# Optimization experiments

Measured on AMD Instinct MI355X. Metric: run time of the kernel, lower is better.

## Reference

```python
import jax, jax.numpy as jnp
import numpy as np

H = 1024
V = 5000
NUM_LAYERS = 2
B, T, U = 2, 128, 64


def setup_inputs() -> dict:
    key = jax.random.key(0)
    ks = jax.random.split(key, 16)
    s = 0.02
    inp = {
        "encoder_out": jax.random.normal(ks[0], (B, T, H), dtype=jnp.float32),
        "targets": jax.random.randint(ks[1], (B, U), 0, V),
        "embed": jax.random.normal(ks[2], (V, H), dtype=jnp.float32) * s,
        # stacked 2-layer LSTM params, PyTorch gate order (i, f, g, o)
        "lstm_Wih": jax.random.normal(ks[3], (NUM_LAYERS, 4 * H, H), dtype=jnp.float32) * s,
        "lstm_Whh": jax.random.normal(ks[4], (NUM_LAYERS, 4 * H, H), dtype=jnp.float32) * s,
        "lstm_bih": jnp.zeros((NUM_LAYERS, 4 * H), dtype=jnp.float32),
        "lstm_bhh": jnp.zeros((NUM_LAYERS, 4 * H), dtype=jnp.float32),
        "enc_W": jax.random.normal(ks[5], (H, H), dtype=jnp.float32) * s,
        "enc_b": jnp.zeros((H,), dtype=jnp.float32),
        "pred_W": jax.random.normal(ks[6], (H, H), dtype=jnp.float32) * s,
        "pred_b": jnp.zeros((H,), dtype=jnp.float32),
        "out_W": jax.random.normal(ks[7], (V + 1, H), dtype=jnp.float32) * s,
        "out_b": jnp.zeros((V + 1,), dtype=jnp.float32),
    }
    return inp


def _lstm_layer(x, Wih, Whh, bih, bhh):
    # x: [B, U, H] -> [B, U, H]; single LSTM layer, PyTorch gate order i,f,g,o
    b, u, h = x.shape
    bias = bih + bhh  # [4H]
    # precompute input projections for all timesteps: [U, B, 4H]
    xg = jnp.einsum('buh,gh->ubg', x, Wih) + bias

    def step(carry, xt):
        hprev, cprev = carry
        gates = xt + hprev @ Whh.T  # [B, 4H]
        i, f, g, o = jnp.split(gates, 4, axis=-1)
        i = jax.nn.sigmoid(i)
        f = jax.nn.sigmoid(f)
        g = jnp.tanh(g)
        o = jax.nn.sigmoid(o)
        c = f * cprev + i * g
        hnew = o * jnp.tanh(c)
        return (hnew, c), hnew

    init = (jnp.zeros((b, h), x.dtype), jnp.zeros((b, h), x.dtype))
    _, hs = jax.lax.scan(step, init, xg)  # hs: [U, B, H]
    return hs.transpose(1, 0, 2)


def reference(encoder_out, targets, embed, lstm_Wih, lstm_Whh, lstm_bih, lstm_bhh,
              enc_W, enc_b, pred_W, pred_b, out_W, out_b):
    # Prediction network: embedding + 2-layer LSTM (deterministic -> no dropout)
    x = embed[targets]  # [B, U, H]
    for l in range(NUM_LAYERS):
        x = _lstm_layer(x, lstm_Wih[l], lstm_Whh[l], lstm_bih[l], lstm_bhh[l])
    pred_out = x  # [B, U, H]

    # Joint network: proj + broadcast add over (T, U) + ReLU + output linear
    enc_p = jnp.einsum('bth,oh->bto', encoder_out, enc_W) + enc_b  # [B, T, H]
    prd_p = jnp.einsum('buh,oh->buo', pred_out, pred_W) + pred_b    # [B, U, H]
    joint = jax.nn.relu(enc_p[:, :, None, :] + prd_p[:, None, :, :])  # [B, T, U, H]
    logits = jnp.einsum('btuh,vh->btuv', joint, out_W) + out_b  # [B, T, U, V+1]
    return logits
```

## Files before the change

kernel.cpp:

```cpp
#include <hip/hip_runtime.h>
#include <hip/hip_bf16.h>

#define B_ 2
#define T_ 128
#define U_ 64
#define H_ 1024
#define NO_ 5001

typedef __attribute__((ext_vector_type(8))) short bf16x8;
typedef __attribute__((ext_vector_type(4))) float f32x4;

__device__ __forceinline__ float bf2f(unsigned short s) {
  unsigned int u = ((unsigned int)s) << 16;
  float f; __builtin_memcpy(&f, &u, 4); return f;
}
__device__ __forceinline__ unsigned short f2bf(float f) {
  unsigned int u; __builtin_memcpy(&u, &f, 4);
  u = u + 0x7FFFu + ((u >> 16) & 1u);
  return (unsigned short)(u >> 16);
}
__device__ __forceinline__ float fsig(float x) {
  x = fminf(fmaxf(x, -30.f), 30.f);
  float e = __expf(-x);
  return __builtin_amdgcn_rcpf(1.f + e);
}
__device__ __forceinline__ float ftanh(float x) {
  x = fminf(fmaxf(x, -15.f), 15.f);
  float e = __expf(2.f * x);
  return (e - 1.f) * __builtin_amdgcn_rcpf(e + 1.f);
}

__device__ __forceinline__ void gload_lds16(const unsigned short* g, unsigned short* l) {
  __builtin_amdgcn_global_load_lds(
      (const __attribute__((address_space(1))) unsigned int*)g,
      (__attribute__((address_space(3))) unsigned int*)l,
      16, 0, 0);
}

#define R_OUTW 1280256
#define R_WIH  (R_OUTW + 2097152)
#define R_WHH  (R_WIH + 2097152)
#define R_ENCW (R_WHH + 262144)
#define R_PRDW (R_ENCW + 262144)
#define R_ENC  (R_PRDW + 65536)
#define R_BIAS (R_ENC + 1280)
#define R_EMB  (R_BIAS + 32768)

__global__ void k_cvt_all(
    const float* __restrict__ outW, const float* __restrict__ Wih,
    const float* __restrict__ Whh,  const float* __restrict__ encW,
    const float* __restrict__ prdW, const float* __restrict__ enc,
    const float* __restrict__ outB,
    const int* __restrict__ tg, const float* __restrict__ em,
    unsigned short* __restrict__ outW_bf, unsigned short* __restrict__ Wih_bf,
    unsigned short* __restrict__ Whh_bf,  unsigned short* __restrict__ encW_bf,
    unsigned short* __restrict__ prdW_bf, unsigned short* __restrict__ enc_bf,
    float* __restrict__ biasPad, unsigned short* __restrict__ x0_bf)
{
  int i = blockIdx.x * 256 + threadIdx.x;
  const float* src; unsigned short* dst; int off;
  if (i < R_OUTW)      { src = outW; dst = outW_bf; off = i; }
  else if (i < R_WIH)  { src = Wih;  dst = Wih_bf;  off = i - R_OUTW; }
  else if (i < R_WHH)  { src = Whh;  dst = Whh_bf;  off = i - R_WIH; }
  else if (i < R_ENCW) { src = encW; dst = encW_bf; off = i - R_WHH; }
  else if (i < R_PRDW) { src = prdW; dst = prdW_bf; off = i - R_ENCW; }
  else if (i < R_ENC)  { src = enc;  dst = enc_bf;  off = i - R_PRDW; }
  else if (i < R_BIAS) {
    int e0 = (i - R_ENC) * 4;
    float4 v;
    v.x = (e0 + 0 < NO_) ? outB[e0 + 0] : 0.f;
    v.y = (e0 + 1 < NO_) ? outB[e0 + 1] : 0.f;
    v.z = (e0 + 2 < NO_) ? outB[e0 + 2] : 0.f;
    v.w = (e0 + 3 < NO_) ? outB[e0 + 3] : 0.f;
    *(float4*)&biasPad[e0] = v;
    return;
  } else {
    int idx = i - R_BIAS;
    int bu = idx >> 8;
    int kc = (idx & 255) << 2;
    int t = tg[bu];
    const float4 v = *(const float4*)&em[(long)t * H_ + kc];
    ushort4 o; o.x = f2bf(v.x); o.y = f2bf(v.y); o.z = f2bf(v.z); o.w = f2bf(v.w);
    *(ushort4*)&x0_bf[bu * H_ + kc] = o;
    return;
  }
  const float4 v = ((const float4*)src)[off];
  ushort4 o;
  o.x = f2bf(v.x); o.y = f2bf(v.y); o.z = f2bf(v.z); o.w = f2bf(v.w);
  ((ushort4*)dst)[off] = o;
}

__global__ __launch_bounds__(256) void gemm_proj(
    const unsigned short* __restrict__ enc_bf, const unsigned short* __restrict__ x2_bf,
    const unsigned short* __restrict__ encW_bf, const unsigned short* __restrict__ prdW_bf,
    const float* __restrict__ encB, const float* __restrict__ prdB,
    float* __restrict__ ep, float* __restrict__ pp)
{
  __shared__ unsigned short As[128 * 32];
  __shared__ unsigned short Bs[128 * 32];
  const int tid = threadIdx.x;
  const unsigned short* A; const unsigned short* W; const float* b1; float* C;
  int m0;
  if (blockIdx.y < 2) { A = enc_bf; W = encW_bf; b1 = encB; C = ep; m0 = blockIdx.y * 128; }
  else                { A = x2_bf;  W = prdW_bf; b1 = prdB; C = pp; m0 = 0; }
  const int n0 = blockIdx.x * 128;
  const int K = H_, N = H_;
  const int lane = tid & 63, w = tid >> 6;
  const int wr = (w >> 1) * 64, wc = (w & 1) * 64;
  const int lr = lane & 15, lk = (lane >> 4) * 8;
  f32x4 acc[4][4] = {};

  for (int k0 = 0; k0 < K; k0 += 32) {
#pragma unroll
    for (int s = 0; s < 2; ++s) {
      int idx = (w * 2 + s) * 64 + lane;
      int row = idx >> 2, c8 = (idx & 3) * 8;
      gload_lds16(&A[(long)(m0 + row) * K + k0 + c8], &As[(w * 2 + s) * 512]);
      gload_lds16(&W[(long)(n0 + row) * K + k0 + c8], &Bs[(w * 2 + s) * 512]);
    }
    __syncthreads();
    bf16x8 aF[4], bF[4];
#pragma unroll
    for (int i = 0; i < 4; ++i) {
      aF[i] = *(const bf16x8*)&As[(wr + i * 16 + lr) * 32 + lk];
      bF[i] = *(const bf16x8*)&Bs[(wc + i * 16 + lr) * 32 + lk];
    }
#pragma unroll
    for (int i = 0; i < 4; ++i)
#pragma unroll
      for (int j = 0; j < 4; ++j)
        acc[i][j] = __builtin_amdgcn_mfma_f32_16x16x32_bf16(aF[i], bF[j], acc[i][j], 0, 0, 0);
    __syncthreads();
  }

  const int lq = (lane >> 4) * 4;
#pragma unroll
  for (int j = 0; j < 4; ++j) {
    int col = n0 + wc + j * 16 + lr;
    float bb = b1[col];
#pragma unroll
    for (int i = 0; i < 4; ++i) {
      int rowg = m0 + wr + i * 16 + lq;
#pragma unroll
      for (int r = 0; r < 4; ++r)
        C[(long)(rowg + r) * N + col] = acc[i][j][r] + bb;
    }
  }
}

#define STAGE_A(kt2, kh, rb) \
  gload_lds16(aSrc[rb] + (kt2) * 64 + (kh) * 32, \
              &As_f[((((kt2) & 1) * 2 + (kh)) * 8192) + ((rb) * 128 + wv * 16) * 32])
#define STAGE_B(kt2, kh, rb) \
  gload_lds16(bSrc[rb] + (kt2) * 64 + (kh) * 32, \
              &Bs_f[((((kt2) & 1) * 2 + (kh)) * 8192) + ((rb) * 128 + wv * 16) * 32])

__global__ __launch_bounds__(512, 1) void gemm_logits(
    const unsigned short* __restrict__ A, const unsigned short* __restrict__ W,
    const float* __restrict__ biasPad, float* __restrict__ C, int M, int N, int K)
{
  __shared__ __align__(16) unsigned short lds_all[65536];
  unsigned short* As_f = lds_all;
  unsigned short* Bs_f = lds_all + 32768;
  const int tid = threadIdx.x;
  const int lane = tid & 63, wv = tid >> 6;
  const int wm = wv >> 2, wn = wv & 3;
  int swzb = (blockIdx.x & 7) * 160 + (blockIdx.x >> 3);
  const int n0 = (swzb >> 6) * 256;
  const int m0 = (swzb & 63) * 256;
  const int NT = K / 64;

  const unsigned short* aSrc[2];
  const unsigned short* bSrc[2];
#pragma unroll
  for (int rb = 0; rb < 2; ++rb) {
    int rl = rb * 128 + (tid >> 2);
    int c2s = (tid & 3) ^ ((rl >> 1) & 3);
    aSrc[rb] = A + (long)(m0 + rl) * K + c2s * 8;
    bSrc[rb] = W + (long)(n0 + rl) * K + c2s * 8;
  }
  int aOff[8], bOff[4];
#pragma unroll
  for (int i = 0; i < 8; ++i) {
    int r = wm * 128 + i * 16 + (lane & 15);
    aOff[i] = r * 32 + (((lane >> 4) ^ ((r >> 1) & 3)) * 8);
  }
#pragma unroll
  for (int j = 0; j < 4; ++j) {
    int r = wn * 64 + j * 16 + (lane & 15);
    bOff[j] = r * 32 + (((lane >> 4) ^ ((r >> 1) & 3)) * 8);
  }

  f32x4 acc[8][4] = {};

  STAGE_A(0, 0, 0); STAGE_A(0, 0, 1); STAGE_B(0, 0, 0); STAGE_B(0, 0, 1);
  STAGE_A(0, 1, 0); STAGE_A(0, 1, 1); STAGE_B(0, 1, 0); STAGE_B(0, 1, 1);

  for (int kt = 0; kt < NT; ++kt) {
    const int b = kt & 1;
    asm volatile("s_waitcnt vmcnt(4)" ::: "memory");
    __builtin_amdgcn_s_barrier();
    __builtin_amdgcn_sched_barrier(0);
    {
      const int base = (b * 2 + 0) * 8192;
      bf16x8 aF[8], bF[4];
#pragma unroll
      for (int i = 0; i < 8; ++i) aF[i] = *(const bf16x8*)&As_f[base + aOff[i]];
#pragma unroll
      for (int j = 0; j < 4; ++j) bF[j] = *(const bf16x8*)&Bs_f[base + bOff[j]];
      if (kt + 1 < NT) {
        STAGE_A(kt + 1, 0, 0); STAGE_A(kt + 1, 0, 1);
        STAGE_B(kt + 1, 0, 0); STAGE_B(kt + 1, 0, 1);
        STAGE_A(kt + 1, 1, 0); STAGE_A(kt + 1, 1, 1);
      }
      __builtin_amdgcn_s_setprio(1);
#pragma unroll
      for (int i = 0; i < 8; ++i)
#pragma unroll
        for (int j = 0; j < 4; ++j)
          acc[i][j] = __builtin_amdgcn_mfma_f32_16x16x32_bf16(aF[i], bF[j], acc[i][j], 0, 0, 0);
      __builtin_amdgcn_s_setprio(0);
    }
    if (kt + 1 < NT) { asm volatile("s_waitcnt vmcnt(6)" ::: "memory"); }
    else             { asm volatile("s_waitcnt vmcnt(0)" ::: "memory"); }
    __builtin_amdgcn_s_barrier();
    __builtin_amdgcn_sched_barrier(0);
    {
      const int base = (b * 2 + 1) * 8192;
      bf16x8 aF[8], bF[4];
#pragma unroll
      for (int i = 0; i < 8; ++i) aF[i] = *(const bf16x8*)&As_f[base + aOff[i]];
#pragma unroll
      for (int j = 0; j < 4; ++j) bF[j] = *(const bf16x8*)&Bs_f[base + bOff[j]];
      if (kt + 1 < NT) { STAGE_B(kt + 1, 1, 0); STAGE_B(kt + 1, 1, 1); }
      __builtin_amdgcn_s_setprio(1);
#pragma unroll
      for (int i = 0; i < 8; ++i)
#pragma unroll
        for (int j = 0; j < 4; ++j)
          acc[i][j] = __builtin_amdgcn_mfma_f32_16x16x32_bf16(aF[i], bF[j], acc[i][j], 0, 0, 0);
      __builtin_amdgcn_s_setprio(0);
    }
  }

  float* eb = (float*)lds_all;
  const int lq = (lane >> 4) * 4;
  float bv4[4];
#pragma unroll
  for (int j = 0; j < 4; ++j) bv4[j] = biasPad[n0 + wn * 64 + j * 16 + (lane & 15)];

#pragma unroll
  for (int cp = 0; cp < 4; ++cp) {
    __syncthreads();
#pragma unroll
    for (int ii = 0; ii < 2; ++ii) {
      int rbase = wm * 32 + ii * 16 + lq;
#pragma unroll
      for (int j = 0; j < 4; ++j) {
        int col = wn * 64 + j * 16 + (lane & 15);
#pragma unroll
        for (int r = 0; r < 4; ++r)
          eb[(rbase + r) * 261 + col] = acc[cp * 2 + ii][j][r] + bv4[j];
      }
    }
    __syncthreads();
    {
      int rl = tid >> 3, ci = tid & 7;
      long grow = (long)m0 + (rl >> 5) * 128 + cp * 32 + (rl & 31);
      float* crow = C + grow * N + n0;
      const float* er = &eb[rl * 261];
#pragma unroll
      for (int k = 0; k < 8; ++k) {
        int col = ci * 4 + k * 32;
        float4 v = *(const float4*)&er[col];
        int gc = n0 + col;
        if (gc + 4 <= N) {
          *(float4*)&crow[col] = v;
        } else if (gc < N) {
          float tmp[4] = {v.x, v.y, v.z, v.w};
#pragma unroll
          for (int e = 0; e < 4; ++e)
            if (gc + e < N) crow[col + e] = tmp[e];
        }
      }
    }
  }
}

__global__ void k_joint(const float* __restrict__ ep, const float* __restrict__ pp,
                        unsigned short* __restrict__ jt)
{
  int idx = blockIdx.x * 256 + threadIdx.x;
  int m = idx >> 8;
  int kc = (idx & 255) << 2;
  int erow = m >> 6;
  int prow = (m >> 13) * U_ + (m & 63);
  const float4 e = *(const float4*)&ep[erow * H_ + kc];
  const float4 p = *(const float4*)&pp[prow * H_ + kc];
  float4 s;
  s.x = fmaxf(e.x + p.x, 0.f); s.y = fmaxf(e.y + p.y, 0.f);
  s.z = fmaxf(e.z + p.z, 0.f); s.w = fmaxf(e.w + p.w, 0.f);
  ushort4 o; o.x = f2bf(s.x); o.y = f2bf(s.y); o.z = f2bf(s.z); o.w = f2bf(s.w);
  *(ushort4*)&jt[m * H_ + kc] = o;
}

__global__ __launch_bounds__(256, 1) void lstm_fused3(
    const unsigned short* __restrict__ x0_bf,
    const unsigned short* __restrict__ Whh0,
    const unsigned short* __restrict__ Wih0,
    const unsigned short* __restrict__ Whh1,
    const unsigned short* __restrict__ Wih1,
    const float* __restrict__ bih0, const float* __restrict__ bhh0,
    const float* __restrict__ bih1, const float* __restrict__ bhh1,
    unsigned short* __restrict__ x2_bf,
    float* __restrict__ hbuf0,
    float* __restrict__ hbuf1,
    float* __restrict__ xbuf,
    float* __restrict__ xg1buf, int* __restrict__ flags1,
    float* __restrict__ xg0buf, int* __restrict__ flags0)
{
  __shared__ float hs[2][H_];
  __shared__ float part[2][4][64][2];
  __shared__ float biasS[64];

  const int tid = threadIdx.x;
  const int grp = blockIdx.x >> 6;
  const int bid = blockIdx.x & 63;
  const int w = tid >> 6, l = tid & 63;
  const int g = l >> 4, q = l & 15;
  const int row = g * 1024 + bid * 16 + q;
  const int kb = w * 256;

#define DOT_BODY(WREG, SRC)                                                              \
  _Pragma("unroll")                                                                      \
  for (int it = 0; it < 32; ++it) {                                                      \
    bf16x8 wv = WREG[it];                                                                \
    float4 h0a = *(const float4*)&SRC[0][kb + it * 8];                                   \
    float4 h0b = *(const float4*)&SRC[0][kb + it * 8 + 4];                               \
    float4 h1a = *(const float4*)&SRC[1][kb + it * 8];                                   \
    float4 h1b = *(const float4*)&SRC[1][kb + it * 8 + 4];                               \
    a00 += bf2f((unsigned short)wv[0]) * h0a.x + bf2f((unsigned short)wv[4]) * h0b.x;    \
    a01 += bf2f((unsigned short)wv[1]) * h0a.y + bf2f((unsigned short)wv[5]) * h0b.y;    \
    a02 += bf2f((unsigned short)wv[2]) * h0a.z + bf2f((unsigned short)wv[6]) * h0b.z;    \
    a03 += bf2f((unsigned short)wv[3]) * h0a.w + bf2f((unsigned short)wv[7]) * h0b.w;    \
    a10 += bf2f((unsigned short)wv[0]) * h1a.x + bf2f((unsigned short)wv[4]) * h1b.x;    \
    a11 += bf2f((unsigned short)wv[1]) * h1a.y + bf2f((unsigned short)wv[5]) * h1b.y;    \
    a12 += bf2f((unsigned short)wv[2]) * h1a.z + bf2f((unsigned short)wv[6]) * h1b.z;    \
    a13 += bf2f((unsigned short)wv[3]) * h1a.w + bf2f((unsigned short)wv[7]) * h1b.w;    \
  }

  if (grp == 0 || grp == 2) {
    const unsigned short* Whh = (grp == 0) ? Whh0 : Whh1;
    float* hbuf   = (grp == 0) ? hbuf0 : hbuf1;
    const float* xgbufR = (grp == 0) ? xg0buf : xg1buf;
    const int* flagsR   = (grp == 0) ? flags0 : flags1;
    bf16x8 wreg[32];
#pragma unroll
    for (int it = 0; it < 32; ++it)
      wreg[it] = *(const bf16x8*)&Whh[(long)row * H_ + kb + it * 8];
    __syncthreads();

    float creg = 0.f;
    for (int u = 0; u < U_; ++u) {
      const int p = u & 1;
      float xgi = 0.f, xgf = 0.f, xgg = 0.f, xgo = 0.f;
      if (tid < 32) {
        const int* fp = &flagsR[(u * 64 + bid) * 16];
        int fv;
        for (;;) {
          asm volatile("global_load_dword %0, %1, off sc1\n\ts_waitcnt vmcnt(0)"
                       : "=v"(fv) : "v"(fp) : "memory");
          if (fv != 0) break;
          __builtin_amdgcn_s_sleep(8);
        }
        const float* xb = &xgbufR[((u * 64 + bid) * 2 + (tid >> 4)) * 64];
        int qq = tid & 15;
        asm volatile("global_load_dword %0, %1, off sc1" : "=&v"(xgi) : "v"(xb + qq) : "memory");
        asm volatile("global_load_dword %0, %1, off sc1" : "=&v"(xgf) : "v"(xb + 16 + qq) : "memory");
        asm volatile("global_load_dword %0, %1, off sc1" : "=&v"(xgg) : "v"(xb + 32 + qq) : "memory");
        asm volatile("global_load_dword %0, %1, off sc1" : "=&v"(xgo) : "v"(xb + 48 + qq) : "memory");
      }
      float a00 = 0.f, a01 = 0.f, a02 = 0.f, a03 = 0.f;
      float a10 = 0.f, a11 = 0.f, a12 = 0.f, a13 = 0.f;
      if (u > 0) {
        const float thr = 4.0f * u - 2.0f;
        const float* base = hbuf + (u & 1) * 2 * H_;
        const float* pa = base + tid * 4;
        const float* pb = base + H_ + tid * 4;
        float4 va, vb;
        for (;;) {
          asm volatile("global_load_dwordx4 %0, %2, off sc1\n\t"
                       "global_load_dwordx4 %1, %3, off sc1\n\t"
                       "s_waitcnt vmcnt(0)"
                       : "=v"(va), "=v"(vb) : "v"(pa), "v"(pb) : "memory");
          if (va.x > thr && va.y > thr && va.z > thr && va.w > thr &&
              vb.x > thr && vb.y > thr && vb.z > thr && vb.w > thr) break;
          __builtin_amdgcn_s_sleep(8);
        }
        const float off = 4.0f * u;
        va.x -= off; va.y -= off; va.z -= off; va.w -= off;
        vb.x -= off; vb.y -= off; vb.z -= off; vb.w -= off;
        *(float4*)&hs[0][tid * 4] = va;
        *(float4*)&hs[1][tid * 4] = vb;
        DOT_BODY(wreg, hs)
      }
      part[p][w][l][0] = (a00 + a01) + (a02 + a03);
      part[p][w][l][1] = (a10 + a11) + (a12 + a13);
      if (tid < 32) {
        asm volatile("s_waitcnt vmcnt(0)"
                     : "+v"(xgi), "+v"(xgf), "+v"(xgg), "+v"(xgo) :: "memory");
      }
      __syncthreads();
      if (tid < 32) {
        int b = tid >> 4, qq = tid & 15;
        float gi = part[p][0][qq][b] + part[p][1][qq][b] + part[p][2][qq][b]
                 + part[p][3][qq][b] + xgi;
        float gf = part[p][0][16 + qq][b] + part[p][1][16 + qq][b] + part[p][2][16 + qq][b]
                 + part[p][3][16 + qq][b] + xgf;
        float gc = part[p][0][32 + qq][b] + part[p][1][32 + qq][b] + part[p][2][32 + qq][b]
                 + part[p][3][32 + qq][b] + xgg;
        float go = part[p][0][48 + qq][b] + part[p][1][48 + qq][b] + part[p][2][48 + qq][b]
                 + part[p][3][48 + qq][b] + xgo;
        float i_ = fsig(gi), f_ = fsig(gf), g_ = ftanh(gc), o_ = fsig(go);
        creg = f_ * creg + i_ * g_;
        float h = o_ * ftanh(creg);
        int j = bid * 16 + qq;
        if (grp == 0) {
          float tvx = h + 4.0f;
          const float* px = &xbuf[u * 2 * H_ + b * H_ + j];
          asm volatile("global_store_dword %0, %1, off sc1" :: "v"(px), "v"(tvx) : "memory");
        } else {
          x2_bf[(b * U_ + u) * H_ + j] = f2bf(h);
        }
        if (u < U_ - 1) {
          float tv = h + 4.0f * (u + 1);
          const float* pp2 = &hbuf[((u + 1) & 1) * 2 * H_ + b * H_ + j];
          asm volatile("global_store_dword %0, %1, off sc1" :: "v"(pp2), "v"(tv) : "memory");
        }
      }
    }
  } else {
    const bool isX1 = (grp == 1);
    const unsigned short* Wih = isX1 ? Wih1 : Wih0;
    const float* bihp = isX1 ? bih1 : bih0;
    const float* bhhp = isX1 ? bhh1 : bhh0;
    float* xgbufW = isX1 ? xg1buf : xg0buf;
    int* flagsW   = isX1 ? flags1 : flags0;
    bf16x8 wreg[32];
#pragma unroll
    for (int it = 0; it < 32; ++it)
      wreg[it] = *(const bf16x8*)&Wih[(long)row * H_ + kb + it * 8];
    if (tid < 64) {
      int rr = (tid >> 4) * 1024 + bid * 16 + (tid & 15);
      biasS[tid] = bihp[rr] + bhhp[rr];
    }
    __syncthreads();

    for (int u = 0; u < U_; ++u) {
      const int p = u & 1;
      if (isX1) {
        const float* base = xbuf + u * 2 * H_;
        const float* pa = base + tid * 4;
        const float* pb = base + H_ + tid * 4;
        float4 va, vb;
        for (;;) {
          asm volatile("global_load_dwordx4 %0, %2, off sc1\n\t"
                       "global_load_dwordx4 %1, %3, off sc1\n\t"
                       "s_waitcnt vmcnt(0)"
                       : "=v"(va), "=v"(vb) : "v"(pa), "v"(pb) : "memory");
          if (va.x > 2.f && va.y > 2.f && va.z > 2.f && va.w > 2.f &&
              vb.x > 2.f && vb.y > 2.f && vb.z > 2.f && vb.w > 2.f) break;
          __builtin_amdgcn_s_sleep(8);
        }
        va.x -= 4.f; va.y -= 4.f; va.z -= 4.f; va.w -= 4.f;
        vb.x -= 4.f; vb.y -= 4.f; vb.z -= 4.f; vb.w -= 4.f;
        *(float4*)&hs[0][tid * 4] = va;
        *(float4*)&hs[1][tid * 4] = vb;
      } else {
        ushort4 xa = *(const ushort4*)&x0_bf[(0 * U_ + u) * H_ + tid * 4];
        ushort4 xb = *(const ushort4*)&x0_bf[(1 * U_ + u) * H_ + tid * 4];
        float4 va, vb;
        va.x = bf2f(xa.x); va.y = bf2f(xa.y); va.z = bf2f(xa.z); va.w = bf2f(xa.w);
        vb.x = bf2f(xb.x); vb.y = bf2f(xb.y); vb.z = bf2f(xb.z); vb.w = bf2f(xb.w);
        *(float4*)&hs[0][tid * 4] = va;
        *(float4*)&hs[1][tid * 4] = vb;
      }

      float a00 = 0.f, a01 = 0.f, a02 = 0.f, a03 = 0.f;
      float a10 = 0.f, a11 = 0.f, a12 = 0.f, a13 = 0.f;
      DOT_BODY(wreg, hs)
      part[p][w][l][0] = (a00 + a01) + (a02 + a03);
      part[p][w][l][1] = (a10 + a11) + (a12 + a13);
      __syncthreads();
      if (tid < 128) {
        int b = tid >> 6, ll = tid & 63;
        float s = part[p][0][ll][b] + part[p][1][ll][b] + part[p][2][ll][b]
                + part[p][3][ll][b] + biasS[ll];
        const float* pw = &xgbufW[((u * 64 + bid) * 2 + b) * 64 + ll];
        asm volatile("global_store_dword %0, %1, off sc1" :: "v"(pw), "v"(s) : "memory");
        asm volatile("s_waitcnt vmcnt(0)" ::: "memory");
      }
      __syncthreads();
      if (tid == 0) {
        int one = 1;
        const int* fp = &flagsW[(u * 64 + bid) * 16];
        asm volatile("global_store_dword %0, %1, off sc1" :: "v"(fp), "v"(one) : "memory");
      }
    }
  }
#undef DOT_BODY
}

extern "C" void kernel_launch(void* const* d_in, const int* in_sizes, int n_in,
                              void* d_out, int out_size, void* d_ws, size_t ws_size,
                              hipStream_t stream)
{
  const float* enc   = (const float*)d_in[0];
  const int*   tg    = (const int*)d_in[1];
  const float* em    = (const float*)d_in[2];
  const float* Wih   = (const float*)d_in[3];
  const float* Whh   = (const float*)d_in[4];
  const float* bih   = (const float*)d_in[5];
  const float* bhh   = (const float*)d_in[6];
  const float* encW  = (const float*)d_in[7];
  const float* encB  = (const float*)d_in[8];
  const float* prdW  = (const float*)d_in[9];
  const float* prdB  = (const float*)d_in[10];
  const float* outW  = (const float*)d_in[11];
  const float* outB  = (const float*)d_in[12];
  float* out = (float*)d_out;
  char* ws = (char*)d_ws;

  unsigned short* outW_bf = (unsigned short*)(ws + 0);
  unsigned short* Wih_bf  = (unsigned short*)(ws + 10485760);
  unsigned short* Whh_bf  = (unsigned short*)(ws + 27262976);
  unsigned short* encW_bf = (unsigned short*)(ws + 44040192);
  unsigned short* prdW_bf = (unsigned short*)(ws + 46137344);
  unsigned short* enc_bf  = (unsigned short*)(ws + 48234496);
  unsigned short* x0_bf   = (unsigned short*)(ws + 48758784);
  unsigned short* x2_bf   = (unsigned short*)(ws + 49283072);
  float* xg1buf = (float*)(ws + 49545216);
  float* hbufL0 = (float*)(ws + 51642368);
  unsigned short* jt = (unsigned short*)(ws + 51659008);
  int*   flags0 = (int*)(ws + 51659008);
  float* xg0buf = (float*)(ws + 51921152);
  float* hbufL1 = (float*)(ws + 85213440);
  float* biasPad = (float*)(ws + 85229824);
  float* xbuf = (float*)(ws + 85250304);
  int* flags1 = (int*)(ws + 85774592);
  float* ep = (float*)(ws + 49545216);
  float* pp = (float*)(ws + 49545216 + 1048576);

  hipMemsetAsync(hbufL0, 0, 16384, stream);
  hipMemsetAsync(hbufL1, 0, 86036736 - 85213440, stream);
  hipMemsetAsync(flags0, 0, 262144, stream);

  k_cvt_all<<<R_EMB / 256, 256, 0, stream>>>(
      outW, Wih, Whh, encW, prdW, enc, outB, tg, em,
      outW_bf, Wih_bf, Whh_bf, encW_bf, prdW_bf, enc_bf, biasPad, x0_bf);

  lstm_fused3<<<256, 256, 0, stream>>>(
      x0_bf,
      Whh_bf, Wih_bf,
      Whh_bf + 4096 * H_, Wih_bf + 4096 * H_,
      bih, bhh, bih + 4096, bhh + 4096,
      x2_bf, hbufL0, hbufL1, xbuf,
      xg1buf, flags1, xg0buf, flags0);

  gemm_proj<<<dim3(8, 3), 256, 0, stream>>>(enc_bf, x2_bf, encW_bf, prdW_bf,
                                            encB, prdB, ep, pp);

  k_joint<<<16384, 256, 0, stream>>>(ep, pp, jt);
  gemm_logits<<<1280, 512, 0, stream>>>(jt, outW_bf, biasPad, out, B_ * T_ * U_, NO_, H_);
}
```

Before: 595.9 us.

## Use MFMA bf16 for recurrent Whh matvec in fused LSTM kernel

Replaces the scalar FP32 dot-product recurrent matvec with MFMA 16x16x32 bf16 instructions. Each wave now owns one gate's 16 rows, so the cross-wave partial-sum reduction is dropped. The hidden state is converted to bf16 in shared memory, with only 2 of 16 MFMA columns active for the batch dimension. The spin-wait sleep is also removed. This lowers the precision of h in the recurrence and adds an extra barrier per step.

```diff
diff --git a/kernel.cpp b/kernel.cpp
--- a/kernel.cpp
+++ b/kernel.cpp
@@ -321,6 +321,8 @@
 {
   __shared__ float hs[2][H_];
   __shared__ float part[2][4][64][2];
+  __shared__ unsigned short hbf[2][H_];
+  __shared__ float gateS[4][2][16];
   __shared__ float biasS[64];
 
   const int tid = threadIdx.x;
@@ -354,15 +356,21 @@
     float* hbuf   = (grp == 0) ? hbuf0 : hbuf1;
     const float* xgbufR = (grp == 0) ? xg0buf : xg1buf;
     const int* flagsR   = (grp == 0) ? flags0 : flags1;
-    bf16x8 wreg[32];
-#pragma unroll
-    for (int it = 0; it < 32; ++it)
-      wreg[it] = *(const bf16x8*)&Whh[(long)row * H_ + kb + it * 8];
+    bf16x8 wfrag[32];
+    {
+      const long arow = (long)(w * 1024 + bid * 16 + (l & 15)) * H_;
+      const int klo = (l >> 4) * 8;
+#pragma unroll
+      for (int kt = 0; kt < 32; ++kt)
+        wfrag[kt] = *(const bf16x8*)&Whh[arow + kt * 32 + klo];
+    }
+    const int klo = (l >> 4) * 8;
+    const bool bactive = (l & 15) < 2;
+    const unsigned short* hrow = &hbf[l & 15][klo];
     __syncthreads();
 
     float creg = 0.f;
     for (int u = 0; u < U_; ++u) {
-      const int p = u & 1;
       float xgi = 0.f, xgf = 0.f, xgg = 0.f, xgo = 0.f;
       if (tid < 32) {
         const int* fp = &flagsR[(u * 64 + bid) * 16];
@@ -380,8 +388,6 @@
         asm volatile("global_load_dword %0, %1, off sc1" : "=&v"(xgg) : "v"(xb + 32 + qq) : "memory");
         asm volatile("global_load_dword %0, %1, off sc1" : "=&v"(xgo) : "v"(xb + 48 + qq) : "memory");
       }
-      float a00 = 0.f, a01 = 0.f, a02 = 0.f, a03 = 0.f;
-      float a10 = 0.f, a11 = 0.f, a12 = 0.f, a13 = 0.f;
       if (u > 0) {
         const float thr = 4.0f * u - 2.0f;
         const float* base = hbuf + (u & 1) * 2 * H_;
@@ -395,17 +401,34 @@
                        : "=v"(va), "=v"(vb) : "v"(pa), "v"(pb) : "memory");
           if (va.x > thr && va.y > thr && va.z > thr && va.w > thr &&
               vb.x > thr && vb.y > thr && vb.z > thr && vb.w > thr) break;
-          __builtin_amdgcn_s_sleep(8);
         }
         const float off = 4.0f * u;
-        va.x -= off; va.y -= off; va.z -= off; va.w -= off;
-        vb.x -= off; vb.y -= off; vb.z -= off; vb.w -= off;
-        *(float4*)&hs[0][tid * 4] = va;
-        *(float4*)&hs[1][tid * 4] = vb;
-        DOT_BODY(wreg, hs)
-      }
-      part[p][w][l][0] = (a00 + a01) + (a02 + a03);
-      part[p][w][l][1] = (a10 + a11) + (a12 + a13);
+        ushort4 ha, hb2;
+        ha.x = f2bf(va.x - off); ha.y = f2bf(va.y - off);
+        ha.z = f2bf(va.z - off); ha.w = f2bf(va.w - off);
+        hb2.x = f2bf(vb.x - off); hb2.y = f2bf(vb.y - off);
+        hb2.z = f2bf(vb.z - off); hb2.w = f2bf(vb.w - off);
+        *(ushort4*)&hbf[0][tid * 4] = ha;
+        *(ushort4*)&hbf[1][tid * 4] = hb2;
+      }
+      __syncthreads();
+      f32x4 acc = {0.f, 0.f, 0.f, 0.f};
+      if (u > 0) {
+        bf16x8 zero8 = {};
+#pragma unroll
+        for (int kt = 0; kt < 32; ++kt) {
+          bf16x8 bF = zero8;
+          if (bactive) bF = *(const bf16x8*)&hrow[kt * 32];
+          acc = __builtin_amdgcn_mfma_f32_16x16x32_bf16(wfrag[kt], bF, acc, 0, 0, 0);
+        }
+      }
+      if (bactive) {
+        int b = l & 15;
+        int r0 = (l >> 4) * 4;
+#pragma unroll
+        for (int r = 0; r < 4; ++r)
+          gateS[w][b][r0 + r] = acc[r];
+      }
       if (tid < 32) {
         asm volatile("s_waitcnt vmcnt(0)"
                      : "+v"(xgi), "+v"(xgf), "+v"(xgg), "+v"(xgo) :: "memory");
@@ -413,14 +436,10 @@
       __syncthreads();
       if (tid < 32) {
         int b = tid >> 4, qq = tid & 15;
-        float gi = part[p][0][qq][b] + part[p][1][qq][b] + part[p][2][qq][b]
-                 + part[p][3][qq][b] + xgi;
-        float gf = part[p][0][16 + qq][b] + part[p][1][16 + qq][b] + part[p][2][16 + qq][b]
-                 + part[p][3][16 + qq][b] + xgf;
-        float gc = part[p][0][32 + qq][b] + part[p][1][32 + qq][b] + part[p][2][32 + qq][b]
-                 + part[p][3][32 + qq][b] + xgg;
-        float go = part[p][0][48 + qq][b] + part[p][1][48 + qq][b] + part[p][2][48 + qq][b]
-                 + part[p][3][48 + qq][b] + xgo;
+        float gi = gateS[0][b][qq] + xgi;
+        float gf = gateS[1][b][qq] + xgf;
+        float gc = gateS[2][b][qq] + xgg;
+        float go = gateS[3][b][qq] + xgo;
         float i_ = fsig(gi), f_ = fsig(gf), g_ = ftanh(gc), o_ = fsig(go);
         creg = f_ * creg + i_ * g_;
         float h = o_ * ftanh(creg);
```

Result: slower. 657.0 us (+10.3%).
